# Kernel tuning notes

Hardware: AMD Instinct MI355X
Metric: run time of the kernel (lower is better)

The kernel has to match this reference:

```python
import jax, jax.numpy as jnp
import numpy as np

B, T, S, D, H = 16, 128, 128, 512, 100

def setup_inputs() -> dict:
    key = jax.random.key(0)
    ks = jax.random.split(key, 10)
    sc = 0.02
    return {
        "input": jax.random.normal(ks[0], (B, T, D), dtype=jnp.float32),
        "memory_bank": jax.random.normal(ks[1], (B, S, D), dtype=jnp.float32),
        "W_in": jax.random.normal(ks[2], (D, D), dtype=jnp.float32) * sc,   # linear_in, no bias
        "W1": jax.random.normal(ks[3], (H, 2 * D), dtype=jnp.float32) * sc,  # linear_1
        "b1": jnp.zeros((H,), dtype=jnp.float32),
        "W2": jax.random.normal(ks[4], (H, H), dtype=jnp.float32) * sc,      # linear_2
        "b2": jnp.zeros((H,), dtype=jnp.float32),
        "w_mean": jax.random.normal(ks[5], (H,), dtype=jnp.float32) * sc,    # mean_out
        "b_mean": jnp.zeros((1,), dtype=jnp.float32),
        "w_var": jax.random.normal(ks[6], (H,), dtype=jnp.float32) * sc,     # var_out
        "b_var": jnp.zeros((1,), dtype=jnp.float32),
        "W_out": jax.random.normal(ks[7], (D, 2 * D), dtype=jnp.float32) * sc,  # linear_out, no bias
    }


def reference(input, memory_bank, W_in, W1, b1, W2, b2, w_mean, b_mean, w_var, b_var, W_out):
    d = input.shape[-1]
    # score(): linear_in(h_t) then bmm with h_s^T -> [B,T,S]
    ht = jnp.einsum('btd,ed->bte', input, W_in)
    align = jnp.einsum('bte,bse->bts', ht, memory_bank)
    # softmax over source dim (no memory_lengths -> no mask)
    align_vectors = jax.nn.softmax(align, axis=-1)
    # get_raw_scores(): fused form of cat([h_t_expand, h_s_expand]) @ W1^T
    W1t, W1s = W1[:, :d], W1[:, d:]
    pt = jnp.einsum('btd,hd->bth', input, W1t)        # [B,T,H]
    ps = jnp.einsum('bsd,hd->bsh', memory_bank, W1s)  # [B,S,H]
    h1 = jax.nn.softplus(pt[:, :, None, :] + ps[:, None, :, :] + b1)  # [B,T,S,H]
    h2 = jax.nn.softplus(jnp.einsum('btsh,gh->btsg', h1, W2) + b2)    # [B,T,S,H]
    h_mean = jax.nn.softplus(jnp.einsum('btsg,g->bts', h2, w_mean) + b_mean[0])
    h_var = jax.nn.softplus(jnp.einsum('btsg,g->bts', h2, w_var) + b_var[0])
    # context + output projection + tanh
    c = jnp.einsum('bts,bsd->btd', align_vectors, memory_bank)
    concat_c = jnp.concatenate([c, input], axis=-1)  # [B,T,2D]
    attn_h = jnp.tanh(jnp.einsum('btf,df->btd', concat_c, W_out))
    # multi-step: transpose to [T,B,*]
    attn_h = jnp.transpose(attn_h, (1, 0, 2))
    align_vectors = jnp.transpose(align_vectors, (1, 0, 2))
    return attn_h, align_vectors, h_mean, h_var
```

## Files before the change

### kernel.cpp

```cpp
#include <hip/hip_runtime.h>
#include <math.h>

#define Bn 16
#define Tn 128
#define Sn 128
#define Dn 512
#define Hn 100
#define TT 8

typedef short short8 __attribute__((ext_vector_type(8)));
typedef float f32x4 __attribute__((ext_vector_type(4)));
typedef unsigned short ushort4v __attribute__((ext_vector_type(4)));

__device__ __forceinline__ float softplus_f(float x) {
    return fmaxf(x, 0.0f) + __logf(1.0f + __expf(-fabsf(x)));
}
__device__ __forceinline__ unsigned short f2bf(float f) {
    unsigned u = __float_as_uint(f);
    unsigned r = u + 0x7FFFu + ((u >> 16) & 1u);
    return (unsigned short)(r >> 16);
}
__device__ __forceinline__ float bf2f(unsigned short h) {
    return __uint_as_float(((unsigned)h) << 16);
}
__device__ __forceinline__ unsigned pk2(float a, float b) {
    return (unsigned)f2bf(a) | ((unsigned)f2bf(b) << 16);
}
struct BfPair { unsigned short h, l; };
__device__ __forceinline__ BfPair split2(float x) {
    BfPair p;
    p.h = f2bf(x);
    p.l = f2bf(x - bf2f(p.h));
    return p;
}

__global__ __launch_bounds__(256)
void conv_all(const float* __restrict__ input, const float* __restrict__ mem,
              const float* __restrict__ W_in, const float* __restrict__ W1,
              const float* __restrict__ W_out, const float* __restrict__ W2,
              unsigned short* __restrict__ inh, unsigned short* __restrict__ inl,
              unsigned short* __restrict__ memh, unsigned short* __restrict__ meml,
              unsigned short* __restrict__ winh, unsigned short* __restrict__ winl,
              unsigned short* __restrict__ w1b, unsigned short* __restrict__ woutb,
              unsigned short* __restrict__ w2b, unsigned short* __restrict__ concatb)
{
    long gid = (long)blockIdx.x * 1024 + (long)threadIdx.x * 4;
    if (gid < 1048576) {
        float4 v = *(const float4*)&input[gid];
        BfPair a = split2(v.x), b = split2(v.y), c = split2(v.z), d = split2(v.w);
        ushort4v h = {a.h, b.h, c.h, d.h};
        ushort4v l = {a.l, b.l, c.l, d.l};
        *(ushort4v*)&inh[gid] = h;
        *(ushort4v*)&inl[gid] = l;
        long row = gid >> 9; int col = (int)(gid & 511);
        *(ushort4v*)&concatb[row * 1024 + 512 + col] = h;
    } else if (gid < 2097152) {
        long e = gid - 1048576;
        float4 v = *(const float4*)&mem[e];
        BfPair a = split2(v.x), b = split2(v.y), c = split2(v.z), d = split2(v.w);
        ushort4v h = {a.h, b.h, c.h, d.h};
        ushort4v l = {a.l, b.l, c.l, d.l};
        *(ushort4v*)&memh[e] = h;
        *(ushort4v*)&meml[e] = l;
    } else if (gid < 2359296) {
        long e = gid - 2097152;
        float4 v = *(const float4*)&W_in[e];
        BfPair a = split2(v.x), b = split2(v.y), c = split2(v.z), d = split2(v.w);
        ushort4v h = {a.h, b.h, c.h, d.h};
        ushort4v l = {a.l, b.l, c.l, d.l};
        *(ushort4v*)&winh[e] = h;
        *(ushort4v*)&winl[e] = l;
    } else if (gid < 2461696) {
        long e = gid - 2359296;
        float4 v = *(const float4*)&W1[e];
        ushort4v h = {f2bf(v.x), f2bf(v.y), f2bf(v.z), f2bf(v.w)};
        *(ushort4v*)&w1b[e] = h;
    } else if (gid < 2985984) {
        long e = gid - 2461696;
        float4 v = *(const float4*)&W_out[e];
        ushort4v h = {f2bf(v.x), f2bf(v.y), f2bf(v.z), f2bf(v.w)};
        *(ushort4v*)&woutb[e] = h;
    } else {
        long e = gid - 2985984;
        int n = (int)(e >> 7), k = (int)(e & 127);
        ushort4v h;
        #pragma unroll
        for (int j = 0; j < 4; ++j) {
            int kj = k + j;
            float val = (n < Hn && kj < Hn) ? W2[n * Hn + kj] : 0.0f;
            h[j] = f2bf(val);
        }
        *(ushort4v*)&w2b[n * 128 + k] = h;
    }
}

__global__ __launch_bounds__(256)
void transpose_mem(const float* __restrict__ mem, unsigned short* __restrict__ memTb)
{
    __shared__ float tile[64][65];
    const int d0 = blockIdx.x * 64, s0 = blockIdx.y * 64, b = blockIdx.z;
    const int tid = threadIdx.x;
    const int r = tid >> 2, cb = (tid & 3) * 16;

    const float* src = mem + ((long)b * Sn + s0 + r) * Dn + d0 + cb;
    #pragma unroll
    for (int j = 0; j < 4; ++j) {
        float4 v = *(const float4*)&src[j * 4];
        tile[r][cb + j * 4 + 0] = v.x;
        tile[r][cb + j * 4 + 1] = v.y;
        tile[r][cb + j * 4 + 2] = v.z;
        tile[r][cb + j * 4 + 3] = v.w;
    }
    __syncthreads();
    unsigned short* dst = memTb + ((long)b * Dn + d0 + r) * Sn + s0 + cb;
    #pragma unroll
    for (int j = 0; j < 4; ++j) {
        ushort4v q;
        q.x = f2bf(tile[cb + j * 4 + 0][r]);
        q.y = f2bf(tile[cb + j * 4 + 1][r]);
        q.z = f2bf(tile[cb + j * 4 + 2][r]);
        q.w = f2bf(tile[cb + j * 4 + 3][r]);
        *(ushort4v*)&dst[j * 4] = q;
    }
}

template<int SPLIT, int EPI, int KSPLIT, int BSEL>
__global__ __launch_bounds__(256)
void mfma_gemm2(const unsigned short* __restrict__ Ah, const unsigned short* __restrict__ Al,
                const unsigned short* __restrict__ Bh, const unsigned short* __restrict__ Bl,
                float* __restrict__ C, unsigned short* __restrict__ Cb,
                unsigned short* __restrict__ Cb2, const float* __restrict__ bias,
                int N, int K, int lda, int ldb, int ldc,
                long sA, long sB, long sC, long sKC)
{
    __shared__ __align__(16) unsigned short As_[(SPLIT ? 2 : 1) * 64 * 64];
    __shared__ __align__(16) unsigned short Bs_[(SPLIT ? 2 : 1) * 64 * 64];
    unsigned short* Asl = As_ + 4096;
    unsigned short* Bsl = Bs_ + 4096;

    const int tid = threadIdx.x;
    const int n0 = blockIdx.x * 64;
    const long m0 = (long)blockIdx.y * 64;
    int bz = blockIdx.z, kh = 0;
    if (KSPLIT) { bz = blockIdx.z & 15; kh = blockIdx.z >> 4; }
    Ah += (long)bz * sA;
    Bh += (long)bz * sB;
    if (SPLIT) { Al += (long)bz * sA; Bl += (long)bz * sB; }
    const bool upperB = blockIdx.y >= (gridDim.y >> 1);
    if (BSEL && upperB) Bh += BSEL;

    const int kbeg = KSPLIT ? kh * (K >> 1) : 0;
    const int kend = KSPLIT ? kbeg + (K >> 1) : K;

    const int wid = tid >> 6, lane = tid & 63;
    const int lm = lane & 15, lq = lane >> 4;
    const int wm = wid & 1, wn = wid >> 1;

    const int sr = tid >> 2;
    const int sc = (tid & 3) * 2;
    const bool bok = (n0 + sr) < N;

    f32x4 acc[2][2];
    #pragma unroll
    for (int i = 0; i < 2; ++i)
        #pragma unroll
        for (int j = 0; j < 2; ++j)
            acc[i][j] = (f32x4){0.f, 0.f, 0.f, 0.f};

    for (int k0 = kbeg; k0 < kend; k0 += 64) {
        __syncthreads();
        #pragma unroll
        for (int i = 0; i < 2; ++i) {
            int c = sc + i, p = c ^ (sr & 7);
            *(short8*)&As_[sr * 64 + p * 8] =
                *(const short8*)&Ah[(m0 + sr) * lda + k0 + c * 8];
            if (SPLIT)
                *(short8*)&Asl[sr * 64 + p * 8] =
                    *(const short8*)&Al[(m0 + sr) * lda + k0 + c * 8];
        }
        #pragma unroll
        for (int i = 0; i < 2; ++i) {
            int c = sc + i, p = c ^ (sr & 7);
            short8 v = {0, 0, 0, 0, 0, 0, 0, 0};
            short8 vl = {0, 0, 0, 0, 0, 0, 0, 0};
            if (bok) {
                v = *(const short8*)&Bh[(long)(n0 + sr) * ldb + k0 + c * 8];
                if (SPLIT) vl = *(const short8*)&Bl[(long)(n0 + sr) * ldb + k0 + c * 8];
            }
            *(short8*)&Bs_[sr * 64 + p * 8] = v;
            if (SPLIT) *(short8*)&Bsl[sr * 64 + p * 8] = vl;
        }
        __syncthreads();
        #pragma unroll
        for (int kst = 0; kst < 2; ++kst) {
            short8 a[2], b[2], a2[2], b2r[2];
            const int pp = (kst * 4 + lq) ^ (lm & 7);
            #pragma unroll
            for (int mt = 0; mt < 2; ++mt) {
                int row = wm * 32 + mt * 16 + lm;
                a[mt] = *(const short8*)&As_[row * 64 + pp * 8];
                if (SPLIT) a2[mt] = *(const short8*)&Asl[row * 64 + pp * 8];
            }
            #pragma unroll
            for (int nt = 0; nt < 2; ++nt) {
                int row = wn * 32 + nt * 16 + lm;
                b[nt] = *(const short8*)&Bs_[row * 64 + pp * 8];
                if (SPLIT) b2r[nt] = *(const short8*)&Bsl[row * 64 + pp * 8];
            }
            #pragma unroll
            for (int mt = 0; mt < 2; ++mt)
                #pragma unroll
                for (int nt = 0; nt < 2; ++nt) {
                    if (SPLIT) {
                        acc[mt][nt] = __builtin_amdgcn_mfma_f32_16x16x32_bf16(
                            a2[mt], b[nt], acc[mt][nt], 0, 0, 0);
                        acc[mt][nt] = __builtin_amdgcn_mfma_f32_16x16x32_bf16(
                            a[mt], b2r[nt], acc[mt][nt], 0, 0, 0);
                    }
                    acc[mt][nt] = __builtin_amdgcn_mfma_f32_16x16x32_bf16(
                        a[mt], b[nt], acc[mt][nt], 0, 0, 0);
                }
        }
    }

    #pragma unroll
    for (int mt = 0; mt < 2; ++mt)
        #pragma unroll
        for (int nt = 0; nt < 2; ++nt)
            #pragma unroll
            for (int r = 0; r < 4; ++r) {
                long m = m0 + wm * 32 + mt * 16 + lq * 4 + r;
                int n = n0 + wn * 32 + nt * 16 + lm;
                float v = acc[mt][nt][r];
                if (EPI == 0) {
                    if (n < N)
                        C[(long)bz * sC + (long)kh * sKC + m * ldc + n] = v;
                } else if (EPI == 1) {
                    unsigned short h = f2bf(v);
                    Cb[m * ldc + n] = h;
                    Cb2[m * ldc + n] = f2bf(v - bf2f(h));
                } else if (EPI == 2) {
                    long bb = m >> 7, tt = m & 127;
                    C[tt * (Bn * Dn) + bb * Dn + n] = tanhf(v);
                } else if (EPI == 3) {
                    Cb[(long)bz * sC + m * ldc + n] = f2bf(v);
                } else {
                    float bb = (!upperB && n < Hn) ? bias[n] : 0.f;
                    C[m * ldc + n] = v + bb;
                }
            }
}

__global__ __launch_bounds__(128)
void softmax_k(const float* __restrict__ a0, const float* __restrict__ a1,
               float* __restrict__ av_out, unsigned short* __restrict__ avb)
{
    const int bt = blockIdx.x;
    const int b = bt >> 7, t = bt & 127;
    const int s = threadIdx.x;
    float v = a0[(long)bt * Sn + s] + a1[(long)bt * Sn + s];

    float m = v;
    #pragma unroll
    for (int o = 32; o > 0; o >>= 1) m = fmaxf(m, __shfl_xor(m, o));
    __shared__ float red[2];
    if ((s & 63) == 0) red[s >> 6] = m;
    __syncthreads();
    m = fmaxf(red[0], red[1]);

    float e = __expf(v - m);
    float sum = e;
    #pragma unroll
    for (int o = 32; o > 0; o >>= 1) sum += __shfl_xor(sum, o);
    __shared__ float red2[2];
    if ((s & 63) == 0) red2[s >> 6] = sum;
    __syncthreads();
    float inv = 1.0f / (red2[0] + red2[1]);

    float av = e * inv;
    av_out[(long)t * (Bn * Sn) + b * Sn + s] = av;
    avb[(long)bt * Sn + s] = f2bf(av);
}

__global__ __launch_bounds__(256)
void mlp_mfma3(const float* __restrict__ ptps,
               const unsigned short* __restrict__ w2b,
               const float* __restrict__ b2,
               const float* __restrict__ w_mean, const float* __restrict__ b_mean,
               const float* __restrict__ w_var, const float* __restrict__ b_var,
               float* __restrict__ mean_out, float* __restrict__ var_out)
{
    __shared__ __align__(16) unsigned short h1s[64 * 128];
    __shared__ __align__(16) unsigned short w2s[112 * 128];
    __shared__ float ptl[TT][128];
    __shared__ float b2p[112], wmp[112], wvp[112];

    const int tg = blockIdx.x;
    const int b  = blockIdx.y >> 1;
    const int s0 = (blockIdx.y & 1) * 64;
    const int tid = threadIdx.x;

    #pragma unroll
    for (int i0 = 0; i0 < 7; ++i0) {
        int i = tid + i0 * 256;
        int r = i >> 4, c = i & 15;
        *(short8*)&w2s[r * 128 + (c ^ (r & 7)) * 8] = *(const short8*)&w2b[i * 8];
    }
    {
        int t = tid >> 5, c4 = (tid & 31) * 4;
        *(float4*)&ptl[t][c4] =
            *(const float4*)&ptps[((long)b * Tn + tg * TT + t) * 128 + c4];
    }
    if (tid < 112) {
        b2p[tid] = (tid < Hn) ? b2[tid] : 0.f;
        wmp[tid] = (tid < Hn) ? w_mean[tid] : 0.f;
        wvp[tid] = (tid < Hn) ? w_var[tid] : 0.f;
    }

    const int r = tid >> 2, cb = tid & 3;
    float psreg[32];
    {
        const float* psrow = ptps + (long)(2048 + b * Sn + s0 + r) * 128 + cb * 32;
        #pragma unroll
        for (int i = 0; i < 8; ++i)
            *(float4*)&psreg[i * 4] = *(const float4*)&psrow[i * 4];
    }
    __syncthreads();

    const int wid = tid >> 6, lane = tid & 63;
    const int lm = lane & 15, lq = lane >> 4;
    const float bm = b_mean[0], bv = b_var[0];

    for (int t = 0; t < TT; ++t) {
        #pragma unroll
        for (int i = 0; i < 4; ++i) {
            float4 pa = *(const float4*)&ptl[t][cb * 32 + i * 8];
            float4 pb = *(const float4*)&ptl[t][cb * 32 + i * 8 + 4];
            float x0 = softplus_f(psreg[i * 8 + 0] + pa.x);
            float x1 = softplus_f(psreg[i * 8 + 1] + pa.y);
            float x2 = softplus_f(psreg[i * 8 + 2] + pa.z);
            float x3 = softplus_f(psreg[i * 8 + 3] + pa.w);
            float x4 = softplus_f(psreg[i * 8 + 4] + pb.x);
            float x5 = softplus_f(psreg[i * 8 + 5] + pb.y);
            float x6 = softplus_f(psreg[i * 8 + 6] + pb.z);
            float x7 = softplus_f(psreg[i * 8 + 7] + pb.w);
            uint4 u;
            u.x = pk2(x0, x1); u.y = pk2(x2, x3);
            u.z = pk2(x4, x5); u.w = pk2(x6, x7);
            *(uint4*)&h1s[r * 128 + ((cb * 4 + i) ^ (r & 7)) * 8] = u;
        }
        __syncthreads();

        f32x4 acc[7];
        #pragma unroll
        for (int j = 0; j < 7; ++j) acc[j] = (f32x4){0.f, 0.f, 0.f, 0.f};
        #pragma unroll
        for (int ks = 0; ks < 4; ++ks) {
            const int p = (ks * 4 + lq) ^ (lm & 7);
            short8 a = *(const short8*)&h1s[(wid * 16 + lm) * 128 + p * 8];
            #pragma unroll
            for (int nt = 0; nt < 7; ++nt) {
                short8 bf = *(const short8*)&w2s[(nt * 16 + lm) * 128 + p * 8];
                acc[nt] = __builtin_amdgcn_mfma_f32_16x16x32_bf16(a, bf, acc[nt], 0, 0, 0);
            }
        }

        float sM[4] = {}, sV[4] = {};
        #pragma unroll
        for (int nt = 0; nt < 7; ++nt) {
            int g = nt * 16 + lm;
            float bg = b2p[g], wm_ = wmp[g], wv_ = wvp[g];
            #pragma unroll
            for (int rr = 0; rr < 4; ++rr) {
                float h2 = softplus_f(acc[nt][rr] + bg);
                sM[rr] = fmaf(h2, wm_, sM[rr]);
                sV[rr] = fmaf(h2, wv_, sV[rr]);
            }
        }
        #pragma unroll
        for (int off = 1; off < 16; off <<= 1)
            #pragma unroll
            for (int rr = 0; rr < 4; ++rr) {
                sM[rr] += __shfl_xor(sM[rr], off);
                sV[rr] += __shfl_xor(sV[rr], off);
            }
        if (lm == 0) {
            const long base = ((long)b * Tn + tg * TT + t) * Sn + s0;
            #pragma unroll
            for (int rr = 0; rr < 4; ++rr) {
                int row = wid * 16 + lq * 4 + rr;
                mean_out[base + row] = softplus_f(sM[rr] + bm);
                var_out[base + row]  = softplus_f(sV[rr] + bv);
            }
        }
        __syncthreads();
    }
}

extern "C" void kernel_launch(void* const* d_in, const int* in_sizes, int n_in,
                              void* d_out, int out_size, void* d_ws, size_t ws_size,
                              hipStream_t stream)
{
    (void)in_sizes; (void)n_in; (void)out_size; (void)ws_size;

    const float* input  = (const float*)d_in[0];
    const float* mem    = (const float*)d_in[1];
    const float* W_in   = (const float*)d_in[2];
    const float* W1     = (const float*)d_in[3];
    const float* b1     = (const float*)d_in[4];
    const float* W2     = (const float*)d_in[5];
    const float* b2     = (const float*)d_in[6];
    const float* w_mean = (const float*)d_in[7];
    const float* b_mean = (const float*)d_in[8];
    const float* w_var  = (const float*)d_in[9];
    const float* b_var  = (const float*)d_in[10];
    const float* W_out  = (const float*)d_in[11];

    float* out      = (float*)d_out;
    float* attn_out = out;
    float* av_out   = out + (long)Tn * Bn * Dn;
    float* mean_out = av_out + (long)Tn * Bn * Sn;
    float* var_out  = mean_out + (long)Bn * Tn * Sn;

    char* p = (char*)d_ws;
    unsigned short* inh   = (unsigned short*)p; p += 2097152;
    unsigned short* memh  = (unsigned short*)p; p += 2097152;
    unsigned short* inl   = (unsigned short*)p; p += 2097152;
    unsigned short* meml  = (unsigned short*)p; p += 2097152;
    unsigned short* winh  = (unsigned short*)p; p += 524288;
    unsigned short* winl  = (unsigned short*)p; p += 524288;
    unsigned short* w1b   = (unsigned short*)p; p += 204800;
    unsigned short* woutb = (unsigned short*)p; p += 1048576;
    unsigned short* w2b   = (unsigned short*)p; p += 28672;
    unsigned short* memTb = (unsigned short*)p; p += 2097152;
    unsigned short* hth   = (unsigned short*)p; p += 2097152;
    unsigned short* htl   = (unsigned short*)p; p += 2097152;
    float* ptps           = (float*)p;          p += 2097152;
    float* algn           = (float*)p;          p += 2097152;
    unsigned short* avb   = (unsigned short*)p; p += 524288;
    unsigned short* concatb = (unsigned short*)p; p += 4194304;

    conv_all<<<dim3(2930), 256, 0, stream>>>(
        input, mem, W_in, W1, W_out, W2,
        inh, inl, memh, meml, winh, winl, w1b, woutb, w2b, concatb);
    transpose_mem<<<dim3(Dn / 64, Sn / 64, Bn), 256, 0, stream>>>(mem, memTb);

    mfma_gemm2<1, 1, 0, 0><<<dim3(8, 32), 256, 0, stream>>>(
        inh, inl, winh, winl, nullptr, hth, htl, nullptr,
        Dn, Dn, Dn, Dn, Dn, 0L, 0L, 0L, 0L);

    mfma_gemm2<0, 4, 0, 512><<<dim3(2, 64), 256, 0, stream>>>(
        inh, nullptr, w1b, nullptr, ptps, nullptr, nullptr, b1,
        Hn, Dn, Dn, 2 * Dn, 128, 0L, 0L, 0L, 0L);

    mfma_gemm2<1, 0, 1, 0><<<dim3(2, 2, 32), 256, 0, stream>>>(
        hth, htl, memh, meml, algn, nullptr, nullptr, nullptr,
        Sn, Dn, Dn, Dn, Sn, (long)Tn * Dn, (long)Sn * Dn,
        (long)Tn * Sn, (long)Bn * Tn * Sn);

    softmax_k<<<dim3(Bn * Tn), 128, 0, stream>>>(
        algn, algn + (long)Bn * Tn * Sn, av_out, avb);

    mfma_gemm2<0, 3, 0, 0><<<dim3(8, 2, 16), 256, 0, stream>>>(
        avb, nullptr, memTb, nullptr, nullptr, concatb, nullptr, nullptr,
        Dn, Sn, Sn, Sn, 2 * Dn, (long)Tn * Sn, (long)Dn * Sn,
        (long)Tn * 2 * Dn, 0L);

    mfma_gemm2<0, 2, 0, 0><<<dim3(8, 32), 256, 0, stream>>>(
        concatb, nullptr, woutb, nullptr, attn_out, nullptr, nullptr, nullptr,
        Dn, 2 * Dn, 2 * Dn, 2 * Dn, Dn, 0L, 0L, 0L, 0L);

    mlp_mfma3<<<dim3(Tn / TT, Bn * 2), 256, 0, stream>>>(
        ptps, w2b, b2, w_mean, b_mean, w_var, b_var, mean_out, var_out);
}
```

Baseline: 192.5 us.

## Merge launches, split align GEMM K four ways, shrink MLP time tile

```diff
diff --git a/kernel.cpp b/kernel.cpp
--- a/kernel.cpp
+++ b/kernel.cpp
@@ -1,4 +1,5 @@
 #include <hip/hip_runtime.h>
+#include <hip/hip_bf16.h>
 #include <math.h>
 
 #define Bn 16
@@ -6,7 +7,7 @@
 #define Sn 128
 #define Dn 512
 #define Hn 100
-#define TT 8
+#define TT 2
 
 typedef short short8 __attribute__((ext_vector_type(8)));
 typedef float f32x4 __attribute__((ext_vector_type(4)));
@@ -23,8 +24,9 @@
 __device__ __forceinline__ float bf2f(unsigned short h) {
     return __uint_as_float(((unsigned)h) << 16);
 }
-__device__ __forceinline__ unsigned pk2(float a, float b) {
-    return (unsigned)f2bf(a) | ((unsigned)f2bf(b) << 16);
+__device__ __forceinline__ unsigned pkrn(float a, float b) {
+    __hip_bfloat162 h = __float22bfloat162_rn(float2{a, b});
+    return *reinterpret_cast<unsigned*>(&h);
 }
 struct BfPair { unsigned short h, l; };
 __device__ __forceinline__ BfPair split2(float x) {
@@ -35,16 +37,46 @@
 }
 
 __global__ __launch_bounds__(256)
-void conv_all(const float* __restrict__ input, const float* __restrict__ mem,
-              const float* __restrict__ W_in, const float* __restrict__ W1,
-              const float* __restrict__ W_out, const float* __restrict__ W2,
-              unsigned short* __restrict__ inh, unsigned short* __restrict__ inl,
-              unsigned short* __restrict__ memh, unsigned short* __restrict__ meml,
-              unsigned short* __restrict__ winh, unsigned short* __restrict__ winl,
-              unsigned short* __restrict__ w1b, unsigned short* __restrict__ woutb,
-              unsigned short* __restrict__ w2b, unsigned short* __restrict__ concatb)
-{
-    long gid = (long)blockIdx.x * 1024 + (long)threadIdx.x * 4;
+void conv_trans(const float* __restrict__ input, const float* __restrict__ mem,
+                const float* __restrict__ W_in, const float* __restrict__ W1,
+                const float* __restrict__ W_out, const float* __restrict__ W2,
+                unsigned short* __restrict__ inh, unsigned short* __restrict__ inl,
+                unsigned short* __restrict__ memh, unsigned short* __restrict__ meml,
+                unsigned short* __restrict__ winh, unsigned short* __restrict__ winl,
+                unsigned short* __restrict__ w1b, unsigned short* __restrict__ woutb,
+                unsigned short* __restrict__ w2b, unsigned short* __restrict__ concatb,
+                unsigned short* __restrict__ memTb)
+{
+    __shared__ float tile[64][65];
+    const int bx = blockIdx.x;
+    if (bx >= 2930) {
+        const int b2x = bx - 2930;
+        const int d0 = (b2x & 7) * 64, s0 = ((b2x >> 3) & 1) * 64, b = b2x >> 4;
+        const int tid = threadIdx.x;
+        const int r = tid >> 2, cb = (tid & 3) * 16;
+        const float* src = mem + ((long)b * Sn + s0 + r) * Dn + d0 + cb;
+        #pragma unroll
+        for (int j = 0; j < 4; ++j) {
+            float4 v = *(const float4*)&src[j * 4];
+            tile[r][cb + j * 4 + 0] = v.x;
+            tile[r][cb + j * 4 + 1] = v.y;
+            tile[r][cb + j * 4 + 2] = v.z;
+            tile[r][cb + j * 4 + 3] = v.w;
+        }
+        __syncthreads();
+        unsigned short* dst = memTb + ((long)b * Dn + d0 + r) * Sn + s0 + cb;
+        #pragma unroll
+        for (int j = 0; j < 4; ++j) {
+            ushort4v q;
+            q.x = f2bf(tile[cb + j * 4 + 0][r]);
+            q.y = f2bf(tile[cb + j * 4 + 1][r]);
+            q.z = f2bf(tile[cb + j * 4 + 2][r]);
+            q.w = f2bf(tile[cb + j * 4 + 3][r]);
+            *(ushort4v*)&dst[j * 4] = q;
+        }
+        return;
+    }
+    long gid = (long)bx * 1024 + (long)threadIdx.x * 4;
     if (gid < 1048576) {
         float4 v = *(const float4*)&input[gid];
         BfPair a = split2(v.x), b = split2(v.y), c = split2(v.z), d = split2(v.w);
@@ -94,63 +126,33 @@
     }
 }
 
-__global__ __launch_bounds__(256)
-void transpose_mem(const float* __restrict__ mem, unsigned short* __restrict__ memTb)
-{
-    __shared__ float tile[64][65];
-    const int d0 = blockIdx.x * 64, s0 = blockIdx.y * 64, b = blockIdx.z;
-    const int tid = threadIdx.x;
-    const int r = tid >> 2, cb = (tid & 3) * 16;
-
-    const float* src = mem + ((long)b * Sn + s0 + r) * Dn + d0 + cb;
-    #pragma unroll
-    for (int j = 0; j < 4; ++j) {
-        float4 v = *(const float4*)&src[j * 4];
-        tile[r][cb + j * 4 + 0] = v.x;
-        tile[r][cb + j * 4 + 1] = v.y;
-        tile[r][cb + j * 4 + 2] = v.z;
-        tile[r][cb + j * 4 + 3] = v.w;
-    }
-    __syncthreads();
-    unsigned short* dst = memTb + ((long)b * Dn + d0 + r) * Sn + s0 + cb;
-    #pragma unroll
-    for (int j = 0; j < 4; ++j) {
-        ushort4v q;
-        q.x = f2bf(tile[cb + j * 4 + 0][r]);
-        q.y = f2bf(tile[cb + j * 4 + 1][r]);
-        q.z = f2bf(tile[cb + j * 4 + 2][r]);
-        q.w = f2bf(tile[cb + j * 4 + 3][r]);
-        *(ushort4v*)&dst[j * 4] = q;
-    }
-}
-
 template<int SPLIT, int EPI, int KSPLIT, int BSEL>
-__global__ __launch_bounds__(256)
-void mfma_gemm2(const unsigned short* __restrict__ Ah, const unsigned short* __restrict__ Al,
-                const unsigned short* __restrict__ Bh, const unsigned short* __restrict__ Bl,
-                float* __restrict__ C, unsigned short* __restrict__ Cb,
-                unsigned short* __restrict__ Cb2, const float* __restrict__ bias,
-                int N, int K, int lda, int ldb, int ldc,
-                long sA, long sB, long sC, long sKC)
-{
-    __shared__ __align__(16) unsigned short As_[(SPLIT ? 2 : 1) * 64 * 64];
-    __shared__ __align__(16) unsigned short Bs_[(SPLIT ? 2 : 1) * 64 * 64];
+__device__ __forceinline__
+void gemm_body(int bx, int by, int bz_in, int upperThresh,
+               const unsigned short* __restrict__ Ah, const unsigned short* __restrict__ Al,
+               const unsigned short* __restrict__ Bh, const unsigned short* __restrict__ Bl,
+               float* __restrict__ C, unsigned short* __restrict__ Cb,
+               unsigned short* __restrict__ Cb2, const float* __restrict__ bias,
+               int N, int K, int lda, int ldb, int ldc,
+               long sA, long sB, long sC, long sKC,
+               unsigned short* As_, unsigned short* Bs_)
+{
     unsigned short* Asl = As_ + 4096;
     unsigned short* Bsl = Bs_ + 4096;
 
     const int tid = threadIdx.x;
-    const int n0 = blockIdx.x * 64;
-    const long m0 = (long)blockIdx.y * 64;
-    int bz = blockIdx.z, kh = 0;
-    if (KSPLIT) { bz = blockIdx.z & 15; kh = blockIdx.z >> 4; }
+    const int n0 = bx * 64;
+    const long m0 = (long)by * 64;
+    int bz = bz_in, kh = 0;
+    if (KSPLIT) { bz = bz_in & 15; kh = bz_in >> 4; }
     Ah += (long)bz * sA;
     Bh += (long)bz * sB;
     if (SPLIT) { Al += (long)bz * sA; Bl += (long)bz * sB; }
-    const bool upperB = blockIdx.y >= (gridDim.y >> 1);
-    if (BSEL && upperB) Bh += BSEL;
-
-    const int kbeg = KSPLIT ? kh * (K >> 1) : 0;
-    const int kend = KSPLIT ? kbeg + (K >> 1) : K;
+    const bool upperB = BSEL && (by >= upperThresh);
+    if (upperB) Bh += BSEL;
+
+    const int kbeg = KSPLIT ? kh * (K / KSPLIT) : 0;
+    const int kend = KSPLIT ? kbeg + (K / KSPLIT) : K;
 
     const int wid = tid >> 6, lane = tid & 63;
     const int lm = lane & 15, lq = lane >> 4;
@@ -251,18 +253,57 @@
             }
 }
 
+template<int SPLIT, int EPI, int KSPLIT, int BSEL>
+__global__ __launch_bounds__(256)
+void mfma_gemm3(const unsigned short* __restrict__ Ah, const unsigned short* __restrict__ Al,
+                const unsigned short* __restrict__ Bh, const unsigned short* __restrict__ Bl,
+                float* __restrict__ C, unsigned short* __restrict__ Cb,
+                unsigned short* __restrict__ Cb2, const float* __restrict__ bias,
+                int N, int K, int lda, int ldb, int ldc,
+                long sA, long sB, long sC, long sKC)
+{
+    __shared__ __align__(16) unsigned short As_[(SPLIT ? 2 : 1) * 4096];
+    __shared__ __align__(16) unsigned short Bs_[(SPLIT ? 2 : 1) * 4096];
+    gemm_body<SPLIT, EPI, KSPLIT, BSEL>(blockIdx.x, blockIdx.y, blockIdx.z,
+        (int)(gridDim.y >> 1), Ah, Al, Bh, Bl, C, Cb, Cb2, bias,
+        N, K, lda, ldb, ldc, sA, sB, sC, sKC, As_, Bs_);
+}
+
+__global__ __launch_bounds__(256)
+void gemm_ht_ptps(const unsigned short* __restrict__ inh, const unsigned short* __restrict__ inl,
+                  const unsigned short* __restrict__ winh, const unsigned short* __restrict__ winl,
+                  unsigned short* __restrict__ hth, unsigned short* __restrict__ htl,
+                  const unsigned short* __restrict__ w1b, float* __restrict__ ptps,
+                  const float* __restrict__ b1)
+{
+    __shared__ __align__(16) unsigned short As_[8192];
+    __shared__ __align__(16) unsigned short Bs_[8192];
+    const int id = blockIdx.x;
+    if (id < 256) {
+        gemm_body<1, 1, 0, 0>(id & 7, id >> 3, 0, 0,
+            inh, inl, winh, winl, nullptr, hth, htl, nullptr,
+            Dn, Dn, Dn, Dn, Dn, 0L, 0L, 0L, 0L, As_, Bs_);
+    } else {
+        const int j = id - 256;
+        gemm_body<0, 4, 0, 512>(j & 1, j >> 1, 0, 32,
+            inh, nullptr, w1b, nullptr, ptps, nullptr, nullptr, b1,
+            Hn, Dn, Dn, 2 * Dn, 128, 0L, 0L, 0L, 0L, As_, Bs_);
+    }
+}
+
 __global__ __launch_bounds__(128)
-void softmax_k(const float* __restrict__ a0, const float* __restrict__ a1,
-               float* __restrict__ av_out, unsigned short* __restrict__ avb)
+void softmax_k4(const float* __restrict__ algn, long kstride,
+                float* __restrict__ av_out, unsigned short* __restrict__ avb)
 {
     const int bt = blockIdx.x;
     const int b = bt >> 7, t = bt & 127;
     const int s = threadIdx.x;
-    float v = a0[(long)bt * Sn + s] + a1[(long)bt * Sn + s];
+    const long o = (long)bt * Sn + s;
+    float v = algn[o] + algn[o + kstride] + algn[o + 2 * kstride] + algn[o + 3 * kstride];
 
     float m = v;
     #pragma unroll
-    for (int o = 32; o > 0; o >>= 1) m = fmaxf(m, __shfl_xor(m, o));
+    for (int off = 32; off > 0; off >>= 1) m = fmaxf(m, __shfl_xor(m, off));
     __shared__ float red[2];
     if ((s & 63) == 0) red[s >> 6] = m;
     __syncthreads();
@@ -271,7 +312,7 @@
     float e = __expf(v - m);
     float sum = e;
     #pragma unroll
-    for (int o = 32; o > 0; o >>= 1) sum += __shfl_xor(sum, o);
+    for (int off = 32; off > 0; off >>= 1) sum += __shfl_xor(sum, off);
     __shared__ float red2[2];
     if ((s & 63) == 0) red2[s >> 6] = sum;
     __syncthreads();
@@ -279,11 +320,11 @@
 
     float av = e * inv;
     av_out[(long)t * (Bn * Sn) + b * Sn + s] = av;
-    avb[(long)bt * Sn + s] = f2bf(av);
+    avb[o] = f2bf(av);
 }
 
 __global__ __launch_bounds__(256)
-void mlp_mfma3(const float* __restrict__ ptps,
+void mlp_mfma4(const float* __restrict__ ptps,
                const unsigned short* __restrict__ w2b,
                const float* __restrict__ b2,
                const float* __restrict__ w_mean, const float* __restrict__ b_mean,
@@ -292,7 +333,7 @@
 {
     __shared__ __align__(16) unsigned short h1s[64 * 128];
     __shared__ __align__(16) unsigned short w2s[112 * 128];
-    __shared__ float ptl[TT][128];
+    __shared__ float ptl[TT][140];
     __shared__ float b2p[112], wmp[112], wvp[112];
 
     const int tg = blockIdx.x;
@@ -303,13 +344,13 @@
     #pragma unroll
     for (int i0 = 0; i0 < 7; ++i0) {
         int i = tid + i0 * 256;
-        int r = i >> 4, c = i & 15;
-        *(short8*)&w2s[r * 128 + (c ^ (r & 7)) * 8] = *(const short8*)&w2b[i * 8];
+        int r_ = i >> 4, c_ = i & 15;
+        *(short8*)&w2s[r_ * 128 + (c_ ^ (r_ & 7)) * 8] = *(const short8*)&w2b[i * 8];
     }
     {
-        int t = tid >> 5, c4 = (tid & 31) * 4;
-        *(float4*)&ptl[t][c4] =
-            *(const float4*)&ptps[((long)b * Tn + tg * TT + t) * 128 + c4];
+        int t = tid >> 7, c = tid & 127;
+        ptl[t][c + 4 * (c >> 5)] =
+            ptps[((long)b * Tn + tg * TT + t) * 128 + c];
     }
     if (tid < 112) {
         b2p[tid] = (tid < Hn) ? b2[tid] : 0.f;
@@ -318,12 +359,15 @@
     }
 
     const int r = tid >> 2, cb = tid & 3;
-    float psreg[32];
+    float psreg[4][8];
     {
-        const float* psrow = ptps + (long)(2048 + b * Sn + s0 + r) * 128 + cb * 32;
-        #pragma unroll
-        for (int i = 0; i < 8; ++i)
-            *(float4*)&psreg[i * 4] = *(const float4*)&psrow[i * 4];
+        const float* psrow = ptps + (long)(2048 + b * Sn + s0 + r) * 128;
+        #pragma unroll
+        for (int i = 0; i < 4; ++i) {
+            int col = (cb + 4 * i) * 8;
+            *(float4*)&psreg[i][0] = *(const float4*)&psrow[col];
+            *(float4*)&psreg[i][4] = *(const float4*)&psrow[col + 4];
+        }
     }
     __syncthreads();
 
@@ -334,20 +378,23 @@
     for (int t = 0; t < TT; ++t) {
         #pragma unroll
         for (int i = 0; i < 4; ++i) {
-            float4 pa = *(const float4*)&ptl[t][cb * 32 + i * 8];
-            float4 pb = *(const float4*)&ptl[t][cb * 32 + i * 8 + 4];
-            float x0 = softplus_f(psreg[i * 8 + 0] + pa.x);
-            float x1 = softplus_f(psreg[i * 8 + 1] + pa.y);
-            float x2 = softplus_f(psreg[i * 8 + 2] + pa.z);
-            float x3 = softplus_f(psreg[i * 8 + 3] + pa.w);
-            float x4 = softplus_f(psreg[i * 8 + 4] + pb.x);
-            float x5 = softplus_f(psreg[i * 8 + 5] + pb.y);
-            float x6 = softplus_f(psreg[i * 8 + 6] + pb.z);
-            float x7 = softplus_f(psreg[i * 8 + 7] + pb.w);
+            const int c = cb + 4 * i;
+            const int col = c * 8;
+            const int base = col + 4 * (col >> 5);
+            float4 pa = *(const float4*)&ptl[t][base];
+            float4 pb = *(const float4*)&ptl[t][base + 4];
+            float x0 = softplus_f(psreg[i][0] + pa.x);
+            float x1 = softplus_f(psreg[i][1] + pa.y);
+            float x2 = softplus_f(psreg[i][2] + pa.z);
+            float x3 = softplus_f(psreg[i][3] + pa.w);
+            float x4 = softplus_f(psreg[i][4] + pb.x);
+            float x5 = softplus_f(psreg[i][5] + pb.y);
+            float x6 = softplus_f(psreg[i][6] + pb.z);
+            float x7 = softplus_f(psreg[i][7] + pb.w);
             uint4 u;
-            u.x = pk2(x0, x1); u.y = pk2(x2, x3);
-            u.z = pk2(x4, x5); u.w = pk2(x6, x7);
-            *(uint4*)&h1s[r * 128 + ((cb * 4 + i) ^ (r & 7)) * 8] = u;
+            u.x = pkrn(x0, x1); u.y = pkrn(x2, x3);
+            u.z = pkrn(x4, x5); u.w = pkrn(x6, x7);
+            *(uint4*)&h1s[r * 128 + (c ^ (r & 7)) * 8] = u;
         }
         __syncthreads();
 
@@ -436,40 +483,35 @@
     unsigned short* hth   = (unsigned short*)p; p += 2097152;
     unsigned short* htl   = (unsigned short*)p; p += 2097152;
     float* ptps           = (float*)p;          p += 2097152;
-    float* algn           = (float*)p;          p += 2097152;
+    float* algn           = (float*)p;          p += 4194304;
     unsigned short* avb   = (unsigned short*)p; p += 524288;
     unsigned short* concatb = (unsigned short*)p; p += 4194304;
 
-    conv_all<<<dim3(2930), 256, 0, stream>>>(
+    const long kstride = (long)Bn * Tn * Sn;
+
+    conv_trans<<<dim3(2930 + 256), 256, 0, stream>>>(
         input, mem, W_in, W1, W_out, W2,
-        inh, inl, memh, meml, winh, winl, w1b, woutb, w2b, concatb);
-    transpose_mem<<<dim3(Dn / 64, Sn / 64, Bn), 256, 0, stream>>>(mem, memTb);
-
-    mfma_gemm2<1, 1, 0, 0><<<dim3(8, 32), 256, 0, stream>>>(
-        inh, inl, winh, winl, nullptr, hth, htl, nullptr,
-        Dn, Dn, Dn, Dn, Dn, 0L, 0L, 0L, 0L);
-
-    mfma_gemm2<0, 4, 0, 512><<<dim3(2, 64), 256, 0, stream>>>(
-        inh, nullptr, w1b, nullptr, ptps, nullptr, nullptr, b1,
-        Hn, Dn, Dn, 2 * Dn, 128, 0L, 0L, 0L, 0L);
-
-    mfma_gemm2<1, 0, 1, 0><<<dim3(2, 2, 32), 256, 0, stream>>>(
+        inh, inl, memh, meml, winh, winl, w1b, woutb, w2b, concatb, memTb);
+
+    gemm_ht_ptps<<<dim3(384), 256, 0, stream>>>(
+        inh, inl, winh, winl, hth, htl, w1b, ptps, b1);
+
+    mfma_gemm3<1, 0, 4, 0><<<dim3(2, 2, 64), 256, 0, stream>>>(
         hth, htl, memh, meml, algn, nullptr, nullptr, nullptr,
         Sn, Dn, Dn, Dn, Sn, (long)Tn * Dn, (long)Sn * Dn,
-        (long)Tn * Sn, (long)Bn * Tn * Sn);
-
-    softmax_k<<<dim3(Bn * Tn), 128, 0, stream>>>(
-        algn, algn + (long)Bn * Tn * Sn, av_out, avb);
-
-    mfma_gemm2<0, 3, 0, 0><<<dim3(8, 2, 16), 256, 0, stream>>>(
+        (long)Tn * Sn, kstride);
+
+    softmax_k4<<<dim3(Bn * Tn), 128, 0, stream>>>(algn, kstride, av_out, avb);
+
+    mfma_gemm3<0, 3, 0, 0><<<dim3(8, 2, 16), 256, 0, stream>>>(
         avb, nullptr, memTb, nullptr, nullptr, concatb, nullptr, nullptr,
         Dn, Sn, Sn, Sn, 2 * Dn, (long)Tn * Sn, (long)Dn * Sn,
         (long)Tn * 2 * Dn, 0L);
 
-    mfma_gemm2<0, 2, 0, 0><<<dim3(8, 32), 256, 0, stream>>>(
+    mfma_gemm3<0, 2, 0, 0><<<dim3(8, 32), 256, 0, stream>>>(
         concatb, nullptr, woutb, nullptr, attn_out, nullptr, nullptr, nullptr,
         Dn, 2 * Dn, 2 * Dn, 2 * Dn, Dn, 0L, 0L, 0L, 0L);
 
-    mlp_mfma3<<<dim3(Tn / TT, Bn * 2), 256, 0, stream>>>(
+    mlp_mfma4<<<dim3(Tn / TT, Bn * 2), 256, 0, stream>>>(
         ptps, w2b, b2, w_mean, b_mean, w_var, b_var, mean_out, var_out);
 }
```

Measured after the change: 173.7 us. 1.11x faster.
